# Performance work log

Hardware: AMD Instinct MI355X
Metric: run time of the kernel (lower is better)

## Reference

```python
import jax, jax.numpy as jnp
import numpy as np

N = 20000      # num nodes
E = 200000     # num edges (no self loops; GATConv adds them)
ND = 128       # node_feature_dim
ED = 64        # edge_feature_dim
H = 256        # hidden_dim (= GAT out_channels per head, concat=False)
HEADS = 4
L = 3          # num_gnn_layers


def setup_inputs() -> dict:
    key = jax.random.key(0)
    ks = jax.random.split(key, 24)
    rng = np.random.default_rng(0)
    src = rng.integers(0, N, size=E)
    dst = (src + 1 + rng.integers(0, N - 1, size=E)) % N  # guaranteed no self loops
    edge_index = jnp.asarray(np.stack([src, dst]), dtype=jnp.int32)
    s = 0.05
    inp = {
        'node_features': jax.random.normal(ks[0], (N, ND), jnp.float32),
        'edge_attr': jax.random.normal(ks[1], (E, ED), jnp.float32),
        'enc_w': jax.random.normal(ks[2], (ND, H), jnp.float32) * s,
        'enc_b': jnp.zeros((H,), jnp.float32),
        'edge_enc_w': jax.random.normal(ks[3], (L, ED, H), jnp.float32) * s,
        'edge_enc_b': jnp.zeros((L, H), jnp.float32),
        'gat_w': jax.random.normal(ks[4], (L, H, HEADS * H), jnp.float32) * s,
        'att_src': jax.random.normal(ks[5], (L, HEADS, H), jnp.float32) * s,
        'att_dst': jax.random.normal(ks[6], (L, HEADS, H), jnp.float32) * s,
        'att_edge': jax.random.normal(ks[7], (L, HEADS, H), jnp.float32) * s,
        'lin_edge_w': jax.random.normal(ks[8], (L, 1, HEADS * H), jnp.float32) * s,
        'gat_b': jnp.zeros((L, H), jnp.float32),
        'ln_g': jnp.ones((L, H), jnp.float32),
        'ln_b': jnp.zeros((L, H), jnp.float32),
        'head_w1': jax.random.normal(ks[9], (4, H, H // 2), jnp.float32) * s,
        'head_b1': jnp.zeros((4, H // 2), jnp.float32),
        'head_w2': jax.random.normal(ks[10], (4, H // 2, 1), jnp.float32) * s,
        'head_b2': jnp.zeros((4, 1), jnp.float32),
        'edge_index': edge_index,
    }
    return inp


def _layernorm(x, g, b, eps=1e-5):
    mu = x.mean(-1, keepdims=True)
    v = ((x - mu) ** 2).mean(-1, keepdims=True)
    return g * (x - mu) / jnp.sqrt(v + eps) + b


def _gat_layer(x, src, dst, ew_full, w, a_s_vec, a_d_vec, a_e_vec, lew, bias):
    # x: [N,H]; GATConv(heads=4, concat=False) with scalar edge feature (edge_dim=1)
    xp = (x @ w).reshape(N, HEADS, H)                       # [N,HEADS,H]
    a_s = (xp * a_s_vec).sum(-1)                            # [N,HEADS]
    a_d = (xp * a_d_vec).sum(-1)                            # [N,HEADS]
    ef = (ew_full[:, None] @ lew).reshape(-1, HEADS, H)     # [Etot,HEADS,H]
    a_e = (ef * a_e_vec).sum(-1)                            # [Etot,HEADS]
    logits = jax.nn.leaky_relu(a_s[src] + a_d[dst] + a_e, 0.2)
    m = jax.ops.segment_max(logits, dst, num_segments=N)    # segment softmax over dst
    p = jnp.exp(logits - m[dst])
    ssum = jax.ops.segment_sum(p, dst, num_segments=N)
    alpha = p / ssum[dst]                                   # [Etot,HEADS]
    out = jax.ops.segment_sum(alpha[:, :, None] * xp[src], dst, num_segments=N)
    return out.mean(1) + bias                               # concat=False -> mean over heads


def reference(node_features, edge_attr, enc_w, enc_b, edge_enc_w, edge_enc_b,
              gat_w, att_src, att_dst, att_edge, lin_edge_w, gat_b,
              ln_g, ln_b, head_w1, head_b1, head_w2, head_b2, edge_index):
    src0, dst0 = edge_index[0], edge_index[1]
    loop = jnp.arange(N, dtype=edge_index.dtype)
    src = jnp.concatenate([src0, loop])   # self loops appended (GATConv add_self_loops)
    dst = jnp.concatenate([dst0, loop])
    deg = jax.ops.segment_sum(jnp.ones((E,), node_features.dtype), dst0, num_segments=N)

    x = jax.nn.relu(node_features @ enc_w + enc_b)          # node encoder (dropout: eval)
    for l in range(L):
        ew = (edge_attr @ edge_enc_w[l] + edge_enc_b[l]).mean(-1)  # [E] scalar edge weight
        loop_w = jax.ops.segment_sum(ew, dst0, num_segments=N) / jnp.maximum(deg, 1.0)
        ew_full = jnp.concatenate([ew, loop_w])             # fill_value='mean' for self loops
        h = _gat_layer(x, src, dst, ew_full, gat_w[l], att_src[l], att_dst[l],
                       att_edge[l], lin_edge_w[l], gat_b[l])
        h = _layernorm(h, ln_g[l], ln_b[l])
        x = jax.nn.relu(x + h)
    emb = x                                                 # [N,H]

    # 4 prediction heads vectorized: k in {attrition, engagement, collaboration, anomaly}
    hmid = jax.nn.relu(jnp.einsum('nd,kdh->knh', emb, head_w1) + head_b1[:, None, :])
    o = jnp.einsum('knh,kho->kno', hmid, head_w2) + head_b2[:, None, :]  # [4,N,1]
    attrition = jax.nn.sigmoid(o[0])
    engagement = o[1]
    collaboration = o[2]
    anomaly = jax.nn.sigmoid(o[3])
    return (attrition, engagement, collaboration, anomaly, emb)
```

## Files before the change

kernel.cpp:

```cpp
#include <hip/hip_runtime.h>
#include <math.h>

#define N_NODES 20000
#define N_EDGES 200000
#define NDIM 128
#define EDIM 64
#define HDIM 256
#define HEADS 4
#define NH 1024
#define NLAYERS 3
#define SCAN_NBLK ((N_NODES + 255) / 256)

typedef __attribute__((ext_vector_type(8))) short short8;
typedef __attribute__((ext_vector_type(4))) float floatx4;

__device__ __forceinline__ float b2f(unsigned short u) {
    union { unsigned u; float f; } c; c.u = ((unsigned)u) << 16; return c.f;
}
__device__ __forceinline__ float b2f_lo(unsigned u) {
    union { unsigned u; float f; } c; c.u = u << 16; return c.f;
}
__device__ __forceinline__ float b2f_hi(unsigned u) {
    union { unsigned u; float f; } c; c.u = u & 0xffff0000u; return c.f;
}
__device__ __forceinline__ unsigned short f2b(float f) {
    union { float f; unsigned u; } c; c.f = f;
    unsigned u = c.u;
    return (unsigned short)((u + 0x7FFFu + ((u >> 16) & 1u)) >> 16);
}
__device__ __forceinline__ float lrelu(float v) { return v > 0.f ? v : 0.2f * v; }

__global__ void hist_kernel(const int* __restrict__ dst0, int* __restrict__ cnt) {
    int e = blockIdx.x * 256 + threadIdx.x;
    if (e < N_EDGES) atomicAdd(&cnt[dst0[e]], 1);
}

__global__ void scan_local(const int* __restrict__ cnt, int* __restrict__ row_ptr,
                           int* __restrict__ bsum) {
    __shared__ int wsum[4];
    int tid = threadIdx.x, lane = tid & 63, wid = tid >> 6;
    int n = blockIdx.x * 256 + tid;
    int v = (n < N_NODES) ? cnt[n] : 0;
    int s = v;
    #pragma unroll
    for (int off = 1; off < 64; off <<= 1) {
        int t = __shfl_up(s, off, 64);
        if (lane >= off) s += t;
    }
    if (lane == 63) wsum[wid] = s;
    __syncthreads();
    int woff = 0;
    #pragma unroll
    for (int w = 0; w < 4; w++) if (w < wid) woff += wsum[w];
    if (n < N_NODES) row_ptr[n] = woff + s - v;
    if (tid == 255) bsum[blockIdx.x] = woff + s;
}

__global__ void scan_bsums(int* __restrict__ bsum, int* __restrict__ boff) {
    __shared__ int wsum[2];
    int tid = threadIdx.x, lane = tid & 63, wid = tid >> 6;
    int v = (tid < SCAN_NBLK) ? bsum[tid] : 0;
    int s = v;
    #pragma unroll
    for (int off = 1; off < 64; off <<= 1) {
        int t = __shfl_up(s, off, 64);
        if (lane >= off) s += t;
    }
    if (lane == 63) wsum[wid] = s;
    __syncthreads();
    int woff = (wid == 1) ? wsum[0] : 0;
    if (tid < SCAN_NBLK) boff[tid] = woff + s - v;
    if (tid == SCAN_NBLK - 1) boff[SCAN_NBLK] = woff + s;
}

__global__ void scan_add(int* __restrict__ row_ptr, const int* __restrict__ boff) {
    int n = blockIdx.x * 256 + threadIdx.x;
    if (n < N_NODES) row_ptr[n] += boff[blockIdx.x];
    if (n == 0) row_ptr[N_NODES] = boff[SCAN_NBLK];
}

__global__ __launch_bounds__(256) void fill_ew(const int* __restrict__ src0,
                                               const int* __restrict__ dst0,
                                               const float* __restrict__ edge_attr,
                                               const float* __restrict__ wmean3,
                                               const float* __restrict__ scal3,
                                               const int* __restrict__ row_ptr,
                                               int* __restrict__ fillc,
                                               int* __restrict__ srcCSR,
                                               float* __restrict__ ewCSR4) {
    int e = blockIdx.x * 256 + threadIdx.x;
    if (e >= N_EDGES) return;
    int d = dst0[e];
    int p = atomicAdd(&fillc[d], 1);
    int pos = row_ptr[d] + p;
    srcCSR[pos] = src0[e];
    const float* row = edge_attr + (size_t)e * EDIM;
    float s0 = 0.f, s1 = 0.f, s2 = 0.f;
    #pragma unroll
    for (int dd = 0; dd < EDIM; dd += 4) {
        float4 a  = *(const float4*)(row + dd);
        float4 w0 = *(const float4*)(wmean3 + dd);
        float4 w1 = *(const float4*)(wmean3 + 64 + dd);
        float4 w2 = *(const float4*)(wmean3 + 128 + dd);
        s0 += a.x * w0.x + a.y * w0.y + a.z * w0.z + a.w * w0.w;
        s1 += a.x * w1.x + a.y * w1.y + a.z * w1.z + a.w * w1.w;
        s2 += a.x * w2.x + a.y * w2.y + a.z * w2.z + a.w * w2.w;
    }
    *(float4*)(ewCSR4 + (size_t)pos * 4) =
        make_float4(s0 + scal3[4], s1 + scal3[12], s2 + scal3[20], 0.f);
}

__global__ void transpose_bf(const float* __restrict__ in, unsigned short* __restrict__ out,
                             int K, int Nn, size_t in_bs, size_t out_bs) {
    in += blockIdx.z * in_bs;
    out += blockIdx.z * out_bs;
    __shared__ float sh[32][33];
    int tx = threadIdx.x, ty = threadIdx.y;
    int kb = blockIdx.y * 32, nb = blockIdx.x * 32;
    #pragma unroll
    for (int i = 0; i < 32; i += 8)
        sh[ty + i][tx] = in[(size_t)(kb + ty + i) * Nn + nb + tx];
    __syncthreads();
    #pragma unroll
    for (int i = 0; i < 32; i += 8)
        out[(size_t)(nb + ty + i) * K + kb + tx] = f2b(sh[tx][ty + i]);
}

__global__ void gat_w_prep(const float* __restrict__ in, unsigned short* __restrict__ out) {
    int z = blockIdx.z, l = z >> 2, h = z & 3;
    __shared__ float sh[32][33];
    int tx = threadIdx.x, ty = threadIdx.y;
    int kb = blockIdx.y * 32, db = blockIdx.x * 32;
    const float* src = in + (size_t)l * HDIM * NH + (size_t)h * HDIM;
    unsigned short* dst = out + (size_t)l * HDIM * NH + (size_t)h * HDIM;
    #pragma unroll
    for (int i = 0; i < 32; i += 8)
        sh[ty + i][tx] = src[(size_t)(kb + ty + i) * NH + db + tx];
    __syncthreads();
    #pragma unroll
    for (int i = 0; i < 32; i += 8)
        dst[(size_t)(db + ty + i) * NH + kb + tx] = f2b(0.25f * sh[tx][ty + i]);
}

__global__ void ws_prep(const float* __restrict__ gat_w, const float* __restrict__ att_src,
                        const float* __restrict__ att_dst,
                        float* __restrict__ ws_s, float* __restrict__ ws_d) {
    int l = blockIdx.x >> 2, h = blockIdx.x & 3;
    int k = threadIdx.x;
    const float* wrow = gat_w + (size_t)l * HDIM * NH + (size_t)k * NH + h * HDIM;
    const float* as = att_src + (size_t)l * NH + h * HDIM;
    const float* ad = att_dst + (size_t)l * NH + h * HDIM;
    float s1 = 0.f, s2 = 0.f;
    for (int d = 0; d < HDIM; d += 4) {
        float4 w4 = *(const float4*)(wrow + d);
        float4 a4 = *(const float4*)(as + d);
        float4 b4 = *(const float4*)(ad + d);
        s1 += w4.x * a4.x + w4.y * a4.y + w4.z * a4.z + w4.w * a4.w;
        s2 += w4.x * b4.x + w4.y * b4.y + w4.z * b4.z + w4.w * b4.w;
    }
    ws_s[(size_t)blockIdx.x * HDIM + k] = s1;
    ws_d[(size_t)blockIdx.x * HDIM + k] = s2;
}

__global__ void conv_bf(const float* __restrict__ in, unsigned short* __restrict__ out) {
    int i = blockIdx.x * 256 + threadIdx.x;
    float4 v = ((const float4*)in)[i];
    ushort4 o;
    o.x = f2b(v.x); o.y = f2b(v.y); o.z = f2b(v.z); o.w = f2b(v.w);
    ((ushort4*)out)[i] = o;
}

template <bool RELU, bool BIAS, bool HEAD2>
__global__ __launch_bounds__(256) void gemm_bf16(
    const unsigned short* __restrict__ A, const unsigned short* __restrict__ Bt,
    const float* __restrict__ bias, unsigned short* __restrict__ C,
    int M, int Ntot, int K,
    const float* __restrict__ w2 = nullptr, const float* __restrict__ b2v = nullptr,
    float* __restrict__ outp = nullptr)
{
    __shared__ char lds[16384];
    unsigned short* As = (unsigned short*)lds;
    unsigned short* Bs = (unsigned short*)(lds + 4096);
    unsigned short* Cs = (unsigned short*)lds;

    int Cb = Ntot >> 7;
    int P  = (M + 63) >> 6;
    int d  = blockIdx.x;
    int xcd = d & 7;
    int i5  = d >> 3;
    int p   = xcd + 8 * (i5 / Cb);
    int cblk = i5 % Cb;
    if (p >= P) return;
    int row0 = p * 64;
    int col0 = cblk * 128;

    int tid = threadIdx.x;
    int lane = tid & 63;
    int wid = tid >> 6;
    int wm = (wid >> 1) * 32;
    int wn = (wid & 1) * 64;
    int lm = lane & 15;
    int q8 = (lane >> 4) * 8;
    int q4 = (lane >> 4) * 4;

    floatx4 acc[2][4];
    #pragma unroll
    for (int i = 0; i < 2; i++)
        #pragma unroll
        for (int j = 0; j < 4; j++)
            acc[i][j] = (floatx4)(0.f);

    for (int k0 = 0; k0 < K; k0 += 32) {
        {
            int arow = tid >> 2;
            int acol = (tid & 3) * 8;
            int garow = row0 + arow; if (garow > M - 1) garow = M - 1;
            __builtin_amdgcn_global_load_lds(
                (__attribute__((address_space(1))) const void*)(A + (size_t)garow * K + k0 + acol),
                (__attribute__((address_space(3))) void*)(As + tid * 8), 16, 0, 0);
        }
        #pragma unroll
        for (int r = 0; r < 2; r++) {
            int chunk = tid + r * 256;
            int brow = chunk >> 2;
            int bcol = (chunk & 3) * 8;
            __builtin_amdgcn_global_load_lds(
                (__attribute__((address_space(1))) const void*)(Bt + (size_t)(col0 + brow) * K + k0 + bcol),
                (__attribute__((address_space(3))) void*)(Bs + chunk * 8), 16, 0, 0);
        }
        __syncthreads();
        short8 af[2], bf[4];
        #pragma unroll
        for (int i = 0; i < 2; i++)
            af[i] = *(const short8*)(As + (wm + i * 16 + lm) * 32 + q8);
        #pragma unroll
        for (int j = 0; j < 4; j++)
            bf[j] = *(const short8*)(Bs + (wn + j * 16 + lm) * 32 + q8);
        #pragma unroll
        for (int i = 0; i < 2; i++)
            #pragma unroll
            for (int j = 0; j < 4; j++)
                acc[i][j] = __builtin_amdgcn_mfma_f32_16x16x32_bf16(af[i], bf[j], acc[i][j], 0, 0, 0);
        __syncthreads();
    }

    #pragma unroll
    for (int i = 0; i < 2; i++) {
        #pragma unroll
        for (int j = 0; j < 4; j++) {
            int cl = wn + j * 16 + lm;
            float bv = BIAS ? bias[col0 + cl] : 0.f;
            #pragma unroll
            for (int reg = 0; reg < 4; reg++) {
                int rl = wm + i * 16 + q4 + reg;
                float v = acc[i][j][reg];
                if (BIAS) v += bv;
                if (RELU) v = fmaxf(v, 0.f);
                Cs[rl * 128 + cl] = f2b(v);
            }
        }
    }
    __syncthreads();
    if constexpr (!HEAD2) {
        int row = tid >> 2;
        int seg = (tid & 3) * 32;
        if (row0 + row < M) {
            #pragma unroll
            for (int u = 0; u < 4; u++) {
                int4 v = *(const int4*)(Cs + row * 128 + seg + u * 8);
                *(int4*)(C + (size_t)(row0 + row) * Ntot + col0 + seg + u * 8) = v;
            }
        }
    } else {
        int row = tid >> 2;
        int seg = (tid & 3) * 32;
        int k = col0 >> 7;
        const float* wr = w2 + k * 128;
        const unsigned short* cr = Cs + row * 128 + seg;
        float s = 0.f;
        #pragma unroll
        for (int u = 0; u < 4; u++) {
            int4 v = *(const int4*)(cr + u * 8);
            float4 w0 = *(const float4*)(wr + seg + u * 8);
            float4 w1 = *(const float4*)(wr + seg + u * 8 + 4);
            s += b2f_lo((unsigned)v.x) * w0.x + b2f_hi((unsigned)v.x) * w0.y
               + b2f_lo((unsigned)v.y) * w0.z + b2f_hi((unsigned)v.y) * w0.w;
            s += b2f_lo((unsigned)v.z) * w1.x + b2f_hi((unsigned)v.z) * w1.y
               + b2f_lo((unsigned)v.w) * w1.z + b2f_hi((unsigned)v.w) * w1.w;
        }
        s += __shfl_xor(s, 1, 64);
        s += __shfl_xor(s, 2, 64);
        if ((tid & 3) == 0 && row0 + row < M) {
            s += b2v[k];
            if (k == 0 || k == 3) s = 1.f / (1.f + __expf(-s));
            outp[(size_t)k * N_NODES + row0 + row] = s;
        }
    }
}

__global__ void layer_prep3(const float* __restrict__ edge_enc_w, const float* __restrict__ edge_enc_b,
                            const float* __restrict__ lin_edge_w, const float* __restrict__ att_edge,
                            float* __restrict__ wmean3, float* __restrict__ scal3)
{
    int l = blockIdx.x;
    const float* eew = edge_enc_w + (size_t)l * EDIM * HDIM;
    const float* eeb = edge_enc_b + (size_t)l * HDIM;
    const float* lew = lin_edge_w + (size_t)l * NH;
    const float* ae  = att_edge + (size_t)l * NH;
    float* wm = wmean3 + l * 64;
    float* sc = scal3 + l * 8;
    int tid = threadIdx.x;
    if (tid < 64) {
        float s = 0.f;
        for (int d = 0; d < HDIM; d++) s += eew[tid * HDIM + d];
        wm[tid] = s * (1.f / HDIM);
    } else if (tid < 68) {
        int h = tid - 64;
        float s = 0.f;
        for (int d = 0; d < HDIM; d++) s += lew[h * HDIM + d] * ae[h * HDIM + d];
        sc[h] = s;
    } else if (tid == 68) {
        float s = 0.f;
        for (int d = 0; d < HDIM; d++) s += eeb[d];
        sc[4] = s * (1.f / HDIM);
    }
}

__global__ void loop_weights_all(const float* __restrict__ ewCSR4, const int* __restrict__ row_ptr,
                                 float* __restrict__ loopw3)
{
    int n = blockIdx.x * 256 + threadIdx.x;
    if (n >= N_NODES) return;
    int r0 = row_ptr[n], r1 = row_ptr[n + 1];
    float s0 = 0.f, s1 = 0.f, s2 = 0.f;
    for (int i = r0; i < r1; i++) {
        float4 w = *(const float4*)(ewCSR4 + (size_t)i * 4);
        s0 += w.x; s1 += w.y; s2 += w.z;
    }
    float inv = 1.f / fmaxf((float)(r1 - r0), 1.f);
    loopw3[n] = s0 * inv;
    loopw3[N_NODES + n] = s1 * inv;
    loopw3[2 * N_NODES + n] = s2 * inv;
}

__global__ __launch_bounds__(256) void attn_x(const unsigned short* __restrict__ x_bf,
                                              const float* __restrict__ ws_s,
                                              const float* __restrict__ ws_d,
                                              float* __restrict__ a_s,
                                              float* __restrict__ a_d)
{
    int wid = threadIdx.x >> 6, lane = threadIdx.x & 63;
    int n = blockIdx.x * 4 + wid;
    ushort4 xv = *(const ushort4*)(x_bf + (size_t)n * HDIM + lane * 4);
    float x0 = b2f(xv.x), x1 = b2f(xv.y), x2 = b2f(xv.z), x3 = b2f(xv.w);
    float ss[4], sd[4];
    #pragma unroll
    for (int h = 0; h < 4; h++) {
        float4 s4 = *(const float4*)(ws_s + h * HDIM + lane * 4);
        float4 d4 = *(const float4*)(ws_d + h * HDIM + lane * 4);
        ss[h] = x0 * s4.x + x1 * s4.y + x2 * s4.z + x3 * s4.w;
        sd[h] = x0 * d4.x + x1 * d4.y + x2 * d4.z + x3 * d4.w;
    }
    #pragma unroll
    for (int off = 32; off > 0; off >>= 1)
        #pragma unroll
        for (int h = 0; h < 4; h++) {
            ss[h] += __shfl_xor(ss[h], off, 64);
            sd[h] += __shfl_xor(sd[h], off, 64);
        }
    if (lane == 0) {
        *(float4*)(a_s + n * 4) = make_float4(ss[0], ss[1], ss[2], ss[3]);
        *(float4*)(a_d + n * 4) = make_float4(sd[0], sd[1], sd[2], sd[3]);
    }
}

__global__ __launch_bounds__(256) void gat_agg_fused(
    const unsigned short* __restrict__ x_bf, const float* __restrict__ a_s,
    const float* __restrict__ a_d, const float* __restrict__ loopw,
    const float* __restrict__ scal, const int* __restrict__ row_ptr,
    const int* __restrict__ srcCSR, const float* __restrict__ ewCSR4,
    int l, unsigned short* __restrict__ agg)
{
    int wid = threadIdx.x >> 6, lane = threadIdx.x & 63;
    int n = blockIdx.x * 4 + wid;
    int r0 = row_ptr[n];
    int deg = row_ptr[n + 1] - r0;
    int cnt = deg + 1;

    float4 c4 = *(const float4*)scal;
    float4 as4 = *(const float4*)(a_s + (size_t)n * 4);
    float4 ad4 = *(const float4*)(a_d + (size_t)n * 4);
    float lw = loopw[n];
    float4 zself;
    zself.x = lrelu(as4.x + ad4.x + c4.x * lw);
    zself.y = lrelu(as4.y + ad4.y + c4.y * lw);
    zself.z = lrelu(as4.z + ad4.z + c4.z * lw);
    zself.w = lrelu(as4.w + ad4.w + c4.w * lw);

    auto comp_z = [&](int c0, int& sv, float4& z) {
        int ix = c0 + lane;
        if (ix < deg) {
            sv = srcCSR[r0 + ix];
            float w = ewCSR4[(((size_t)(r0 + ix)) << 2) + l];
            float4 zs = *(const float4*)(a_s + (size_t)sv * 4);
            z.x = lrelu(zs.x + ad4.x + c4.x * w);
            z.y = lrelu(zs.y + ad4.y + c4.y * w);
            z.z = lrelu(zs.z + ad4.z + c4.z * w);
            z.w = lrelu(zs.w + ad4.w + c4.w * w);
        } else if (ix == deg) {
            sv = n; z = zself;
        } else {
            sv = n; z.x = z.y = z.z = z.w = -1e30f;
        }
    };

    int sv0; float4 z0;
    comp_z(0, sv0, z0);
    float4 p0;
    p0.x = __expf(z0.x); p0.y = __expf(z0.y);
    p0.z = __expf(z0.z); p0.w = __expf(z0.w);
    float s0 = p0.x, s1 = p0.y, s2 = p0.z, s3 = p0.w;
    for (int c0 = 64; c0 < cnt; c0 += 64) {
        int sv; float4 z; comp_z(c0, sv, z);
        s0 += __expf(z.x); s1 += __expf(z.y);
        s2 += __expf(z.z); s3 += __expf(z.w);
    }
    #pragma unroll
    for (int off = 32; off > 0; off >>= 1) {
        s0 += __shfl_xor(s0, off, 64);
        s1 += __shfl_xor(s1, off, 64);
        s2 += __shfl_xor(s2, off, 64);
        s3 += __shfl_xor(s3, off, 64);
    }
    float i0 = 1.f / s0, i1 = 1.f / s1, i2 = 1.f / s2, i3 = 1.f / s3;
    float4 al0;
    al0.x = p0.x * i0; al0.y = p0.y * i1; al0.z = p0.z * i2; al0.w = p0.w * i3;

    float acc[4][4] = {};
    const unsigned short* xw = x_bf + (size_t)lane * 4;

    auto acc_one = [&](uint2 u, float a0, float a1, float a2, float a3) {
        float x0 = b2f_lo(u.x), x1 = b2f_hi(u.x), x2 = b2f_lo(u.y), x3 = b2f_hi(u.y);
        acc[0][0] += a0 * x0; acc[0][1] += a0 * x1; acc[0][2] += a0 * x2; acc[0][3] += a0 * x3;
        acc[1][0] += a1 * x0; acc[1][1] += a1 * x1; acc[1][2] += a1 * x2; acc[1][3] += a1 * x3;
        acc[2][0] += a2 * x0; acc[2][1] += a2 * x1; acc[2][2] += a2 * x2; acc[2][3] += a2 * x3;
        acc[3][0] += a3 * x0; acc[3][1] += a3 * x1; acc[3][2] += a3 * x2; acc[3][3] += a3 * x3;
    };

    auto agg_chunk = [&](int sv, float4 al, int mc) {
        int j = 0;
        for (; j + 3 < mc; j += 4) {
            int sA = __builtin_amdgcn_readfirstlane(__shfl(sv, j, 64));
            int sB = __builtin_amdgcn_readfirstlane(__shfl(sv, j + 1, 64));
            int sC = __builtin_amdgcn_readfirstlane(__shfl(sv, j + 2, 64));
            int sD = __builtin_amdgcn_readfirstlane(__shfl(sv, j + 3, 64));
            uint2 uA = *(const uint2*)(xw + (size_t)sA * HDIM);
            uint2 uB = *(const uint2*)(xw + (size_t)sB * HDIM);
            uint2 uC = *(const uint2*)(xw + (size_t)sC * HDIM);
            uint2 uD = *(const uint2*)(xw + (size_t)sD * HDIM);
            acc_one(uA, __shfl(al.x, j, 64), __shfl(al.y, j, 64),
                        __shfl(al.z, j, 64), __shfl(al.w, j, 64));
            acc_one(uB, __shfl(al.x, j + 1, 64), __shfl(al.y, j + 1, 64),
                        __shfl(al.z, j + 1, 64), __shfl(al.w, j + 1, 64));
            acc_one(uC, __shfl(al.x, j + 2, 64), __shfl(al.y, j + 2, 64),
                        __shfl(al.z, j + 2, 64), __shfl(al.w, j + 2, 64));
            acc_one(uD, __shfl(al.x, j + 3, 64), __shfl(al.y, j + 3, 64),
                        __shfl(al.z, j + 3, 64), __shfl(al.w, j + 3, 64));
        }
        for (; j + 1 < mc; j += 2) {
            int sA = __builtin_amdgcn_readfirstlane(__shfl(sv, j, 64));
            int sB = __builtin_amdgcn_readfirstlane(__shfl(sv, j + 1, 64));
            uint2 uA = *(const uint2*)(xw + (size_t)sA * HDIM);
            uint2 uB = *(const uint2*)(xw + (size_t)sB * HDIM);
            acc_one(uA, __shfl(al.x, j, 64), __shfl(al.y, j, 64),
                        __shfl(al.z, j, 64), __shfl(al.w, j, 64));
            acc_one(uB, __shfl(al.x, j + 1, 64), __shfl(al.y, j + 1, 64),
                        __shfl(al.z, j + 1, 64), __shfl(al.w, j + 1, 64));
        }
        if (j < mc) {
            int sA = __builtin_amdgcn_readfirstlane(__shfl(sv, j, 64));
            uint2 uA = *(const uint2*)(xw + (size_t)sA * HDIM);
            acc_one(uA, __shfl(al.x, j, 64), __shfl(al.y, j, 64),
                        __shfl(al.z, j, 64), __shfl(al.w, j, 64));
        }
    };

    agg_chunk(sv0, al0, min(64, cnt));
    for (int c0 = 64; c0 < cnt; c0 += 64) {
        int sv; float4 z; comp_z(c0, sv, z);
        float4 al;
        al.x = __expf(z.x) * i0; al.y = __expf(z.y) * i1;
        al.z = __expf(z.z) * i2; al.w = __expf(z.w) * i3;
        agg_chunk(sv, al, min(64, cnt - c0));
    }

    unsigned short* ag = agg + (size_t)n * NH + lane * 4;
    #pragma unroll
    for (int h = 0; h < 4; h++) {
        ushort4 o;
        o.x = f2b(acc[h][0]); o.y = f2b(acc[h][1]);
        o.z = f2b(acc[h][2]); o.w = f2b(acc[h][3]);
        *(ushort4*)(ag + h * 256) = o;
    }
}

template <bool ATTN, bool EMB>
__global__ __launch_bounds__(256) void ln_residual(const unsigned short* __restrict__ y_bf,
                                                   const float* __restrict__ ln_g,
                                                   const float* __restrict__ ln_b,
                                                   unsigned short* __restrict__ x_bf,
                                                   const float* __restrict__ ws_s,
                                                   const float* __restrict__ ws_d,
                                                   float* __restrict__ a_s,
                                                   float* __restrict__ a_d,
                                                   float* __restrict__ emb_out)
{
    int n = blockIdx.x * 4 + (threadIdx.x >> 6);
    int lane = threadIdx.x & 63;
    ushort4 yv = *(const ushort4*)(y_bf + (size_t)n * HDIM + lane * 4);
    float y0 = b2f(yv.x), y1 = b2f(yv.y), y2 = b2f(yv.z), y3 = b2f(yv.w);
    float s1 = y0 + y1 + y2 + y3;
    float s2 = y0 * y0 + y1 * y1 + y2 * y2 + y3 * y3;
    #pragma unroll
    for (int off = 32; off > 0; off >>= 1) {
        s1 += __shfl_xor(s1, off, 64);
        s2 += __shfl_xor(s2, off, 64);
    }
    float mu = s1 * (1.f / HDIM);
    float var = s2 * (1.f / HDIM) - mu * mu;
    float rsig = rsqrtf(var + 1e-5f);
    float4 g = *(const float4*)(ln_g + lane * 4);
    float4 b = *(const float4*)(ln_b + lane * 4);
    ushort4 xv = *(const ushort4*)(x_bf + (size_t)n * HDIM + lane * 4);
    ushort4 o;
    o.x = f2b(fmaxf(b2f(xv.x) + g.x * (y0 - mu) * rsig + b.x, 0.f));
    o.y = f2b(fmaxf(b2f(xv.y) + g.y * (y1 - mu) * rsig + b.y, 0.f));
    o.z = f2b(fmaxf(b2f(xv.z) + g.z * (y2 - mu) * rsig + b.z, 0.f));
    o.w = f2b(fmaxf(b2f(xv.w) + g.w * (y3 - mu) * rsig + b.w, 0.f));
    *(ushort4*)(x_bf + (size_t)n * HDIM + lane * 4) = o;

    float xn0 = b2f(o.x), xn1 = b2f(o.y), xn2 = b2f(o.z), xn3 = b2f(o.w);
    if (EMB) {
        *(float4*)(emb_out + (size_t)n * HDIM + lane * 4) = make_float4(xn0, xn1, xn2, xn3);
    }
    if (ATTN) {
        float ss[4], sd[4];
        #pragma unroll
        for (int h = 0; h < 4; h++) {
            float4 s4 = *(const float4*)(ws_s + h * HDIM + lane * 4);
            float4 d4 = *(const float4*)(ws_d + h * HDIM + lane * 4);
            ss[h] = xn0 * s4.x + xn1 * s4.y + xn2 * s4.z + xn3 * s4.w;
            sd[h] = xn0 * d4.x + xn1 * d4.y + xn2 * d4.z + xn3 * d4.w;
        }
        #pragma unroll
        for (int off = 32; off > 0; off >>= 1)
            #pragma unroll
            for (int h = 0; h < 4; h++) {
                ss[h] += __shfl_xor(ss[h], off, 64);
                sd[h] += __shfl_xor(sd[h], off, 64);
            }
        if (lane == 0) {
            *(float4*)(a_s + n * 4) = make_float4(ss[0], ss[1], ss[2], ss[3]);
            *(float4*)(a_d + n * 4) = make_float4(sd[0], sd[1], sd[2], sd[3]);
        }
    }
}

extern "C" void kernel_launch(void* const* d_in, const int* in_sizes, int n_in,
                              void* d_out, int out_size, void* d_ws, size_t ws_size,
                              hipStream_t stream) {
    const float* node_features = (const float*)d_in[0];
    const float* edge_attr     = (const float*)d_in[1];
    const float* enc_w         = (const float*)d_in[2];
    const float* enc_b         = (const float*)d_in[3];
    const float* edge_enc_w    = (const float*)d_in[4];
    const float* edge_enc_b    = (const float*)d_in[5];
    const float* gat_w         = (const float*)d_in[6];
    const float* att_src       = (const float*)d_in[7];
    const float* att_dst       = (const float*)d_in[8];
    const float* att_edge      = (const float*)d_in[9];
    const float* lin_edge_w    = (const float*)d_in[10];
    const float* gat_b         = (const float*)d_in[11];
    const float* ln_g          = (const float*)d_in[12];
    const float* ln_b          = (const float*)d_in[13];
    const float* head_w1       = (const float*)d_in[14];
    const float* head_b1       = (const float*)d_in[15];
    const float* head_w2       = (const float*)d_in[16];
    const float* head_b2       = (const float*)d_in[17];
    const int*   edge_index    = (const int*)d_in[18];
    const int* src0 = edge_index;
    const int* dst0 = edge_index + N_EDGES;
    float* out = (float*)d_out;

    char* cur = (char*)d_ws;
    auto alloc = [&](size_t bytes) { char* p = cur; cur += (bytes + 255) & ~(size_t)255; return p; };
    unsigned short* x_bf   = (unsigned short*)alloc((size_t)N_NODES * HDIM * 2);
    unsigned short* agg    = (unsigned short*)alloc((size_t)N_NODES * NH * 2);
    unsigned short* y_bf   = (unsigned short*)alloc((size_t)N_NODES * HDIM * 2);
    unsigned short* nf_bf  = (unsigned short*)alloc((size_t)N_NODES * NDIM * 2);
    unsigned short* enc_wt = (unsigned short*)alloc((size_t)HDIM * NDIM * 2);
    unsigned short* gw2t   = (unsigned short*)alloc((size_t)NLAYERS * NH * HDIM * 2);
    unsigned short* hw1t   = (unsigned short*)alloc((size_t)512 * HDIM * 2);
    float* ws_s   = (float*)alloc((size_t)NLAYERS * 4 * HDIM * 4);
    float* ws_d   = (float*)alloc((size_t)NLAYERS * 4 * HDIM * 4);
    float* a_s    = (float*)alloc((size_t)N_NODES * 4 * 4);
    float* a_d    = (float*)alloc((size_t)N_NODES * 4 * 4);
    float* ewCSR4 = (float*)alloc((size_t)N_EDGES * 4 * 4);
    float* loopw3 = (float*)alloc((size_t)3 * N_NODES * 4);
    float* wmean3 = (float*)alloc(192 * 4);
    float* scal3  = (float*)alloc(24 * 4);
    int* cnt      = (int*)alloc((size_t)2 * N_NODES * 4);
    int* fillc    = cnt + N_NODES;
    int* row_ptr  = (int*)alloc((size_t)(N_NODES + 1) * 4);
    int* bsum     = (int*)alloc((size_t)(SCAN_NBLK + 1) * 4);
    int* boff     = (int*)alloc((size_t)(SCAN_NBLK + 1) * 4);
    int* srcCSR   = (int*)alloc((size_t)N_EDGES * 4);

    hipMemsetAsync(cnt, 0, (size_t)2 * N_NODES * sizeof(int), stream);

    layer_prep3<<<3, 128, 0, stream>>>(edge_enc_w, edge_enc_b, lin_edge_w, att_edge, wmean3, scal3);
    hist_kernel<<<(N_EDGES + 255) / 256, 256, 0, stream>>>(dst0, cnt);
    scan_local<<<SCAN_NBLK, 256, 0, stream>>>(cnt, row_ptr, bsum);
    scan_bsums<<<1, 128, 0, stream>>>(bsum, boff);
    scan_add<<<SCAN_NBLK, 256, 0, stream>>>(row_ptr, boff);
    fill_ew<<<(N_EDGES + 255) / 256, 256, 0, stream>>>(src0, dst0, edge_attr, wmean3, scal3,
                                                       row_ptr, fillc, srcCSR, ewCSR4);
    loop_weights_all<<<(N_NODES + 255) / 256, 256, 0, stream>>>(ewCSR4, row_ptr, loopw3);

    conv_bf<<<(N_NODES * NDIM / 4) / 256, 256, 0, stream>>>(node_features, nf_bf);
    transpose_bf<<<dim3(HDIM / 32, NDIM / 32, 1), dim3(32, 8), 0, stream>>>(
        enc_w, enc_wt, NDIM, HDIM, 0, 0);
    gat_w_prep<<<dim3(8, 8, 12), dim3(32, 8), 0, stream>>>(gat_w, gw2t);
    ws_prep<<<12, 256, 0, stream>>>(gat_w, att_src, att_dst, ws_s, ws_d);
    transpose_bf<<<dim3(128 / 32, HDIM / 32, 4), dim3(32, 8), 0, stream>>>(
        head_w1, hw1t, HDIM, 128, (size_t)HDIM * 128, (size_t)128 * HDIM);

    const int GEMM_GRID_256 = 8 * (((N_NODES + 63) / 64 + 7) / 8) * (256 / 128);
    const int GEMM_GRID_512 = 8 * (((N_NODES + 63) / 64 + 7) / 8) * (512 / 128);

    gemm_bf16<true, true, false><<<GEMM_GRID_256, 256, 0, stream>>>(
        nf_bf, enc_wt, enc_b, x_bf, N_NODES, HDIM, NDIM);
    attn_x<<<N_NODES / 4, 256, 0, stream>>>(x_bf, ws_s, ws_d, a_s, a_d);

    for (int l = 0; l < NLAYERS; l++) {
        gat_agg_fused<<<N_NODES / 4, 256, 0, stream>>>(
            x_bf, a_s, a_d, loopw3 + (size_t)l * N_NODES, scal3 + l * 8,
            row_ptr, srcCSR, ewCSR4, l, agg);
        gemm_bf16<false, true, false><<<GEMM_GRID_256, 256, 0, stream>>>(
            agg, gw2t + (size_t)l * NH * HDIM, gat_b + (size_t)l * HDIM, y_bf,
            N_NODES, HDIM, NH);
        if (l < NLAYERS - 1) {
            ln_residual<true, false><<<N_NODES / 4, 256, 0, stream>>>(
                y_bf, ln_g + (size_t)l * HDIM, ln_b + (size_t)l * HDIM, x_bf,
                ws_s + (size_t)(l + 1) * 4 * HDIM, ws_d + (size_t)(l + 1) * 4 * HDIM,
                a_s, a_d, nullptr);
        } else {
            ln_residual<false, true><<<N_NODES / 4, 256, 0, stream>>>(
                y_bf, ln_g + (size_t)l * HDIM, ln_b + (size_t)l * HDIM, x_bf,
                nullptr, nullptr, nullptr, nullptr, out + 4 * N_NODES);
        }
    }

    gemm_bf16<true, true, true><<<GEMM_GRID_512, 256, 0, stream>>>(
        x_bf, hw1t, head_b1, nullptr, N_NODES, 512, HDIM,
        head_w2, head_b2, out);
}
```

Before: 427.0 us.

## Fuse GEMM with LayerNorm, residual and attention epilogue; single-block scan

Replaces the per-layer GEMM plus separate ln_residual and attn_x kernels with a 32-row-by-256-column GEMM whose epilogue does bias, LayerNorm, residual, ReLU, the attention-score dot products and the embedding write. This removes the y_bf intermediate round trip and several launches. It also replaces the three-kernel prefix scan with one 1024-thread block. The wider full-row tile gives a smaller grid (625 blocks) and uses more LDS per block, and the GEMM now computes in place on x_bf while other blocks read only their own rows.

```diff
diff --git a/kernel.cpp b/kernel.cpp
--- a/kernel.cpp
+++ b/kernel.cpp
@@ -9,7 +9,6 @@
 #define HEADS 4
 #define NH 1024
 #define NLAYERS 3
-#define SCAN_NBLK ((N_NODES + 255) / 256)
 
 typedef __attribute__((ext_vector_type(8))) short short8;
 typedef __attribute__((ext_vector_type(4))) float floatx4;
@@ -35,48 +34,38 @@
     if (e < N_EDGES) atomicAdd(&cnt[dst0[e]], 1);
 }
 
-__global__ void scan_local(const int* __restrict__ cnt, int* __restrict__ row_ptr,
-                           int* __restrict__ bsum) {
-    __shared__ int wsum[4];
-    int tid = threadIdx.x, lane = tid & 63, wid = tid >> 6;
-    int n = blockIdx.x * 256 + tid;
-    int v = (n < N_NODES) ? cnt[n] : 0;
-    int s = v;
+__global__ __launch_bounds__(1024) void scan_full(const int* __restrict__ cnt,
+                                                  int* __restrict__ row_ptr) {
+    const int PER = 20;
+    __shared__ int wtot[16];
+    int t = threadIdx.x, lane = t & 63, wid = t >> 6;
+    int base = t * PER;
+    int loc[PER];
+    int s = 0;
+    #pragma unroll
+    for (int i = 0; i < PER; i++) {
+        int idx = base + i;
+        int v = (idx < N_NODES) ? cnt[idx] : 0;
+        loc[i] = s; s += v;
+    }
+    int inc = s;
     #pragma unroll
     for (int off = 1; off < 64; off <<= 1) {
-        int t = __shfl_up(s, off, 64);
-        if (lane >= off) s += t;
-    }
-    if (lane == 63) wsum[wid] = s;
+        int tt = __shfl_up(inc, off, 64);
+        if (lane >= off) inc += tt;
+    }
+    if (lane == 63) wtot[wid] = inc;
     __syncthreads();
     int woff = 0;
     #pragma unroll
-    for (int w = 0; w < 4; w++) if (w < wid) woff += wsum[w];
-    if (n < N_NODES) row_ptr[n] = woff + s - v;
-    if (tid == 255) bsum[blockIdx.x] = woff + s;
-}
-
-__global__ void scan_bsums(int* __restrict__ bsum, int* __restrict__ boff) {
-    __shared__ int wsum[2];
-    int tid = threadIdx.x, lane = tid & 63, wid = tid >> 6;
-    int v = (tid < SCAN_NBLK) ? bsum[tid] : 0;
-    int s = v;
-    #pragma unroll
-    for (int off = 1; off < 64; off <<= 1) {
-        int t = __shfl_up(s, off, 64);
-        if (lane >= off) s += t;
-    }
-    if (lane == 63) wsum[wid] = s;
-    __syncthreads();
-    int woff = (wid == 1) ? wsum[0] : 0;
-    if (tid < SCAN_NBLK) boff[tid] = woff + s - v;
-    if (tid == SCAN_NBLK - 1) boff[SCAN_NBLK] = woff + s;
-}
-
-__global__ void scan_add(int* __restrict__ row_ptr, const int* __restrict__ boff) {
-    int n = blockIdx.x * 256 + threadIdx.x;
-    if (n < N_NODES) row_ptr[n] += boff[blockIdx.x];
-    if (n == 0) row_ptr[N_NODES] = boff[SCAN_NBLK];
+    for (int w = 0; w < 16; w++) if (w < wid) woff += wtot[w];
+    int excl = woff + inc - s;
+    #pragma unroll
+    for (int i = 0; i < PER; i++) {
+        int idx = base + i;
+        if (idx < N_NODES) row_ptr[idx] = excl + loc[i];
+    }
+    if (t == 1023) row_ptr[N_NODES] = excl + s;
 }
 
 __global__ __launch_bounds__(256) void fill_ew(const int* __restrict__ src0,
@@ -170,13 +159,157 @@
     ((ushort4*)out)[i] = o;
 }
 
-template <bool RELU, bool BIAS, bool HEAD2>
-__global__ __launch_bounds__(256) void gemm_bf16(
+template <bool RELU, bool LN, bool ATTN, bool EMB>
+__global__ __launch_bounds__(256) void gemm_fused(
     const unsigned short* __restrict__ A, const unsigned short* __restrict__ Bt,
-    const float* __restrict__ bias, unsigned short* __restrict__ C,
-    int M, int Ntot, int K,
-    const float* __restrict__ w2 = nullptr, const float* __restrict__ b2v = nullptr,
-    float* __restrict__ outp = nullptr)
+    const float* __restrict__ bias, unsigned short* __restrict__ x_bf, int K,
+    const float* __restrict__ ln_g, const float* __restrict__ ln_b,
+    const float* __restrict__ ws_s, const float* __restrict__ ws_d,
+    float* __restrict__ a_s, float* __restrict__ a_d,
+    float* __restrict__ emb_out)
+{
+    __shared__ char lds[33280];
+    unsigned short* As = (unsigned short*)lds;
+    unsigned short* Bs = (unsigned short*)(lds + 2048);
+    float* Cs = (float*)lds;
+
+    int row0 = blockIdx.x * 32;
+    int tid = threadIdx.x;
+    int lane = tid & 63;
+    int wid = tid >> 6;
+    int wn = wid * 64;
+    int lm = lane & 15;
+    int q8 = (lane >> 4) * 8;
+    int q4 = (lane >> 4) * 4;
+
+    floatx4 acc[2][4];
+    #pragma unroll
+    for (int i = 0; i < 2; i++)
+        #pragma unroll
+        for (int j = 0; j < 4; j++)
+            acc[i][j] = (floatx4)(0.f);
+
+    for (int k0 = 0; k0 < K; k0 += 32) {
+        if (tid < 128) {
+            int arow = tid >> 2;
+            int acol = (tid & 3) * 8;
+            __builtin_amdgcn_global_load_lds(
+                (__attribute__((address_space(1))) const void*)(A + (size_t)(row0 + arow) * K + k0 + acol),
+                (__attribute__((address_space(3))) void*)(As + tid * 8), 16, 0, 0);
+        }
+        #pragma unroll
+        for (int r = 0; r < 4; r++) {
+            int chunk = tid + r * 256;
+            int brow = chunk >> 2;
+            int bcol = (chunk & 3) * 8;
+            __builtin_amdgcn_global_load_lds(
+                (__attribute__((address_space(1))) const void*)(Bt + (size_t)brow * K + k0 + bcol),
+                (__attribute__((address_space(3))) void*)(Bs + chunk * 8), 16, 0, 0);
+        }
+        __syncthreads();
+        short8 af[2], bf[4];
+        #pragma unroll
+        for (int i = 0; i < 2; i++)
+            af[i] = *(const short8*)(As + (i * 16 + lm) * 32 + q8);
+        #pragma unroll
+        for (int j = 0; j < 4; j++)
+            bf[j] = *(const short8*)(Bs + (wn + j * 16 + lm) * 32 + q8);
+        #pragma unroll
+        for (int i = 0; i < 2; i++)
+            #pragma unroll
+            for (int j = 0; j < 4; j++)
+                acc[i][j] = __builtin_amdgcn_mfma_f32_16x16x32_bf16(af[i], bf[j], acc[i][j], 0, 0, 0);
+        __syncthreads();
+    }
+
+    #pragma unroll
+    for (int i = 0; i < 2; i++) {
+        #pragma unroll
+        for (int j = 0; j < 4; j++) {
+            int cl = wn + j * 16 + lm;
+            float bv = bias[cl];
+            #pragma unroll
+            for (int reg = 0; reg < 4; reg++) {
+                int rl = i * 16 + q4 + reg;
+                Cs[rl * 260 + cl] = acc[i][j][reg] + bv;
+            }
+        }
+    }
+    __syncthreads();
+
+    float4 g4, b4;
+    float4 wsv[4], wdv[4];
+    if (LN) {
+        g4 = *(const float4*)(ln_g + lane * 4);
+        b4 = *(const float4*)(ln_b + lane * 4);
+    }
+    if (ATTN) {
+        #pragma unroll
+        for (int h = 0; h < 4; h++) {
+            wsv[h] = *(const float4*)(ws_s + h * HDIM + lane * 4);
+            wdv[h] = *(const float4*)(ws_d + h * HDIM + lane * 4);
+        }
+    }
+    #pragma unroll
+    for (int t = 0; t < 8; t++) {
+        int r = wid * 8 + t;
+        int node = row0 + r;
+        float4 y = *(const float4*)(Cs + r * 260 + lane * 4);
+        float xn0, xn1, xn2, xn3;
+        if (LN) {
+            float s1 = y.x + y.y + y.z + y.w;
+            float s2 = y.x * y.x + y.y * y.y + y.z * y.z + y.w * y.w;
+            #pragma unroll
+            for (int off = 32; off > 0; off >>= 1) {
+                s1 += __shfl_xor(s1, off, 64);
+                s2 += __shfl_xor(s2, off, 64);
+            }
+            float mu = s1 * (1.f / HDIM);
+            float var = s2 * (1.f / HDIM) - mu * mu;
+            float rsig = rsqrtf(var + 1e-5f);
+            ushort4 xv = *(const ushort4*)(x_bf + (size_t)node * HDIM + lane * 4);
+            xn0 = fmaxf(b2f(xv.x) + g4.x * (y.x - mu) * rsig + b4.x, 0.f);
+            xn1 = fmaxf(b2f(xv.y) + g4.y * (y.y - mu) * rsig + b4.y, 0.f);
+            xn2 = fmaxf(b2f(xv.z) + g4.z * (y.z - mu) * rsig + b4.z, 0.f);
+            xn3 = fmaxf(b2f(xv.w) + g4.w * (y.w - mu) * rsig + b4.w, 0.f);
+        } else {
+            xn0 = fmaxf(y.x, 0.f); xn1 = fmaxf(y.y, 0.f);
+            xn2 = fmaxf(y.z, 0.f); xn3 = fmaxf(y.w, 0.f);
+        }
+        ushort4 o;
+        o.x = f2b(xn0); o.y = f2b(xn1); o.z = f2b(xn2); o.w = f2b(xn3);
+        *(ushort4*)(x_bf + (size_t)node * HDIM + lane * 4) = o;
+        float v0 = b2f(o.x), v1 = b2f(o.y), v2 = b2f(o.z), v3 = b2f(o.w);
+        if (EMB) {
+            *(float4*)(emb_out + (size_t)node * HDIM + lane * 4) = make_float4(v0, v1, v2, v3);
+        }
+        if (ATTN) {
+            float ss[4], sd[4];
+            #pragma unroll
+            for (int h = 0; h < 4; h++) {
+                ss[h] = v0 * wsv[h].x + v1 * wsv[h].y + v2 * wsv[h].z + v3 * wsv[h].w;
+                sd[h] = v0 * wdv[h].x + v1 * wdv[h].y + v2 * wdv[h].z + v3 * wdv[h].w;
+            }
+            #pragma unroll
+            for (int off = 32; off > 0; off >>= 1)
+                #pragma unroll
+                for (int h = 0; h < 4; h++) {
+                    ss[h] += __shfl_xor(ss[h], off, 64);
+                    sd[h] += __shfl_xor(sd[h], off, 64);
+                }
+            if (lane == 0) {
+                *(float4*)(a_s + node * 4) = make_float4(ss[0], ss[1], ss[2], ss[3]);
+                *(float4*)(a_d + node * 4) = make_float4(sd[0], sd[1], sd[2], sd[3]);
+            }
+        }
+    }
+}
+
+__global__ __launch_bounds__(256) void gemm_head(
+    const unsigned short* __restrict__ A, const unsigned short* __restrict__ Bt,
+    const float* __restrict__ bias, int M, int Ntot, int K,
+    const float* __restrict__ w2, const float* __restrict__ b2v,
+    float* __restrict__ outp)
 {
     __shared__ char lds[16384];
     unsigned short* As = (unsigned short*)lds;
@@ -249,52 +382,38 @@
         #pragma unroll
         for (int j = 0; j < 4; j++) {
             int cl = wn + j * 16 + lm;
-            float bv = BIAS ? bias[col0 + cl] : 0.f;
+            float bv = bias[col0 + cl];
             #pragma unroll
             for (int reg = 0; reg < 4; reg++) {
                 int rl = wm + i * 16 + q4 + reg;
-                float v = acc[i][j][reg];
-                if (BIAS) v += bv;
-                if (RELU) v = fmaxf(v, 0.f);
+                float v = fmaxf(acc[i][j][reg] + bv, 0.f);
                 Cs[rl * 128 + cl] = f2b(v);
             }
         }
     }
     __syncthreads();
-    if constexpr (!HEAD2) {
-        int row = tid >> 2;
-        int seg = (tid & 3) * 32;
-        if (row0 + row < M) {
-            #pragma unroll
-            for (int u = 0; u < 4; u++) {
-                int4 v = *(const int4*)(Cs + row * 128 + seg + u * 8);
-                *(int4*)(C + (size_t)(row0 + row) * Ntot + col0 + seg + u * 8) = v;
-            }
-        }
-    } else {
-        int row = tid >> 2;
-        int seg = (tid & 3) * 32;
-        int k = col0 >> 7;
-        const float* wr = w2 + k * 128;
-        const unsigned short* cr = Cs + row * 128 + seg;
-        float s = 0.f;
-        #pragma unroll
-        for (int u = 0; u < 4; u++) {
-            int4 v = *(const int4*)(cr + u * 8);
-            float4 w0 = *(const float4*)(wr + seg + u * 8);
-            float4 w1 = *(const float4*)(wr + seg + u * 8 + 4);
-            s += b2f_lo((unsigned)v.x) * w0.x + b2f_hi((unsigned)v.x) * w0.y
-               + b2f_lo((unsigned)v.y) * w0.z + b2f_hi((unsigned)v.y) * w0.w;
-            s += b2f_lo((unsigned)v.z) * w1.x + b2f_hi((unsigned)v.z) * w1.y
-               + b2f_lo((unsigned)v.w) * w1.z + b2f_hi((unsigned)v.w) * w1.w;
-        }
-        s += __shfl_xor(s, 1, 64);
-        s += __shfl_xor(s, 2, 64);
-        if ((tid & 3) == 0 && row0 + row < M) {
-            s += b2v[k];
-            if (k == 0 || k == 3) s = 1.f / (1.f + __expf(-s));
-            outp[(size_t)k * N_NODES + row0 + row] = s;
-        }
+    int row = tid >> 2;
+    int seg = (tid & 3) * 32;
+    int k = col0 >> 7;
+    const float* wr = w2 + k * 128;
+    const unsigned short* cr = Cs + row * 128 + seg;
+    float s = 0.f;
+    #pragma unroll
+    for (int u = 0; u < 4; u++) {
+        int4 v = *(const int4*)(cr + u * 8);
+        float4 w0 = *(const float4*)(wr + seg + u * 8);
+        float4 w1 = *(const float4*)(wr + seg + u * 8 + 4);
+        s += b2f_lo((unsigned)v.x) * w0.x + b2f_hi((unsigned)v.x) * w0.y
+           + b2f_lo((unsigned)v.y) * w0.z + b2f_hi((unsigned)v.y) * w0.w;
+        s += b2f_lo((unsigned)v.z) * w1.x + b2f_hi((unsigned)v.z) * w1.y
+           + b2f_lo((unsigned)v.w) * w1.z + b2f_hi((unsigned)v.w) * w1.w;
+    }
+    s += __shfl_xor(s, 1, 64);
+    s += __shfl_xor(s, 2, 64);
+    if ((tid & 3) == 0 && row0 + row < M) {
+        s += b2v[k];
+        if (k == 0 || k == 3) s = 1.f / (1.f + __expf(-s));
+        outp[(size_t)k * N_NODES + row0 + row] = s;
     }
 }
 
@@ -343,37 +462,6 @@
     loopw3[2 * N_NODES + n] = s2 * inv;
 }
 
-__global__ __launch_bounds__(256) void attn_x(const unsigned short* __restrict__ x_bf,
-                                              const float* __restrict__ ws_s,
-                                              const float* __restrict__ ws_d,
-                                              float* __restrict__ a_s,
-                                              float* __restrict__ a_d)
-{
-    int wid = threadIdx.x >> 6, lane = threadIdx.x & 63;
-    int n = blockIdx.x * 4 + wid;
-    ushort4 xv = *(const ushort4*)(x_bf + (size_t)n * HDIM + lane * 4);
-    float x0 = b2f(xv.x), x1 = b2f(xv.y), x2 = b2f(xv.z), x3 = b2f(xv.w);
-    float ss[4], sd[4];
-    #pragma unroll
-    for (int h = 0; h < 4; h++) {
-        float4 s4 = *(const float4*)(ws_s + h * HDIM + lane * 4);
-        float4 d4 = *(const float4*)(ws_d + h * HDIM + lane * 4);
-        ss[h] = x0 * s4.x + x1 * s4.y + x2 * s4.z + x3 * s4.w;
-        sd[h] = x0 * d4.x + x1 * d4.y + x2 * d4.z + x3 * d4.w;
-    }
-    #pragma unroll
-    for (int off = 32; off > 0; off >>= 1)
-        #pragma unroll
-        for (int h = 0; h < 4; h++) {
-            ss[h] += __shfl_xor(ss[h], off, 64);
-            sd[h] += __shfl_xor(sd[h], off, 64);
-        }
-    if (lane == 0) {
-        *(float4*)(a_s + n * 4) = make_float4(ss[0], ss[1], ss[2], ss[3]);
-        *(float4*)(a_d + n * 4) = make_float4(sd[0], sd[1], sd[2], sd[3]);
-    }
-}
-
 __global__ __launch_bounds__(256) void gat_agg_fused(
     const unsigned short* __restrict__ x_bf, const float* __restrict__ a_s,
     const float* __restrict__ a_d, const float* __restrict__ loopw,
@@ -501,68 +589,6 @@
         o.x = f2b(acc[h][0]); o.y = f2b(acc[h][1]);
         o.z = f2b(acc[h][2]); o.w = f2b(acc[h][3]);
         *(ushort4*)(ag + h * 256) = o;
-    }
-}
-
-template <bool ATTN, bool EMB>
-__global__ __launch_bounds__(256) void ln_residual(const unsigned short* __restrict__ y_bf,
-                                                   const float* __restrict__ ln_g,
-                                                   const float* __restrict__ ln_b,
-                                                   unsigned short* __restrict__ x_bf,
-                                                   const float* __restrict__ ws_s,
-                                                   const float* __restrict__ ws_d,
-                                                   float* __restrict__ a_s,
-                                                   float* __restrict__ a_d,
-                                                   float* __restrict__ emb_out)
-{
-    int n = blockIdx.x * 4 + (threadIdx.x >> 6);
-    int lane = threadIdx.x & 63;
-    ushort4 yv = *(const ushort4*)(y_bf + (size_t)n * HDIM + lane * 4);
-    float y0 = b2f(yv.x), y1 = b2f(yv.y), y2 = b2f(yv.z), y3 = b2f(yv.w);
-    float s1 = y0 + y1 + y2 + y3;
-    float s2 = y0 * y0 + y1 * y1 + y2 * y2 + y3 * y3;
-    #pragma unroll
-    for (int off = 32; off > 0; off >>= 1) {
-        s1 += __shfl_xor(s1, off, 64);
-        s2 += __shfl_xor(s2, off, 64);
-    }
-    float mu = s1 * (1.f / HDIM);
-    float var = s2 * (1.f / HDIM) - mu * mu;
-    float rsig = rsqrtf(var + 1e-5f);
-    float4 g = *(const float4*)(ln_g + lane * 4);
-    float4 b = *(const float4*)(ln_b + lane * 4);
-    ushort4 xv = *(const ushort4*)(x_bf + (size_t)n * HDIM + lane * 4);
-    ushort4 o;
-    o.x = f2b(fmaxf(b2f(xv.x) + g.x * (y0 - mu) * rsig + b.x, 0.f));
-    o.y = f2b(fmaxf(b2f(xv.y) + g.y * (y1 - mu) * rsig + b.y, 0.f));
-    o.z = f2b(fmaxf(b2f(xv.z) + g.z * (y2 - mu) * rsig + b.z, 0.f));
-    o.w = f2b(fmaxf(b2f(xv.w) + g.w * (y3 - mu) * rsig + b.w, 0.f));
-    *(ushort4*)(x_bf + (size_t)n * HDIM + lane * 4) = o;
-
-    float xn0 = b2f(o.x), xn1 = b2f(o.y), xn2 = b2f(o.z), xn3 = b2f(o.w);
-    if (EMB) {
-        *(float4*)(emb_out + (size_t)n * HDIM + lane * 4) = make_float4(xn0, xn1, xn2, xn3);
-    }
-    if (ATTN) {
-        float ss[4], sd[4];
-        #pragma unroll
-        for (int h = 0; h < 4; h++) {
-            float4 s4 = *(const float4*)(ws_s + h * HDIM + lane * 4);
-            float4 d4 = *(const float4*)(ws_d + h * HDIM + lane * 4);
-            ss[h] = xn0 * s4.x + xn1 * s4.y + xn2 * s4.z + xn3 * s4.w;
-            sd[h] = xn0 * d4.x + xn1 * d4.y + xn2 * d4.z + xn3 * d4.w;
-        }
-        #pragma unroll
-        for (int off = 32; off > 0; off >>= 1)
-            #pragma unroll
-            for (int h = 0; h < 4; h++) {
-                ss[h] += __shfl_xor(ss[h], off, 64);
-                sd[h] += __shfl_xor(sd[h], off, 64);
-            }
-        if (lane == 0) {
-            *(float4*)(a_s + n * 4) = make_float4(ss[0], ss[1], ss[2], ss[3]);
-            *(float4*)(a_d + n * 4) = make_float4(sd[0], sd[1], sd[2], sd[3]);
-        }
     }
 }
 
@@ -596,7 +622,6 @@
     auto alloc = [&](size_t bytes) { char* p = cur; cur += (bytes + 255) & ~(size_t)255; return p; };
     unsigned short* x_bf   = (unsigned short*)alloc((size_t)N_NODES * HDIM * 2);
     unsigned short* agg    = (unsigned short*)alloc((size_t)N_NODES * NH * 2);
-    unsigned short* y_bf   = (unsigned short*)alloc((size_t)N_NODES * HDIM * 2);
     unsigned short* nf_bf  = (unsigned short*)alloc((size_t)N_NODES * NDIM * 2);
     unsigned short* enc_wt = (unsigned short*)alloc((size_t)HDIM * NDIM * 2);
     unsigned short* gw2t   = (unsigned short*)alloc((size_t)NLAYERS * NH * HDIM * 2);
@@ -612,17 +637,13 @@
     int* cnt      = (int*)alloc((size_t)2 * N_NODES * 4);
     int* fillc    = cnt + N_NODES;
     int* row_ptr  = (int*)alloc((size_t)(N_NODES + 1) * 4);
-    int* bsum     = (int*)alloc((size_t)(SCAN_NBLK + 1) * 4);
-    int* boff     = (int*)alloc((size_t)(SCAN_NBLK + 1) * 4);
     int* srcCSR   = (int*)alloc((size_t)N_EDGES * 4);
 
     hipMemsetAsync(cnt, 0, (size_t)2 * N_NODES * sizeof(int), stream);
 
     layer_prep3<<<3, 128, 0, stream>>>(edge_enc_w, edge_enc_b, lin_edge_w, att_edge, wmean3, scal3);
     hist_kernel<<<(N_EDGES + 255) / 256, 256, 0, stream>>>(dst0, cnt);
-    scan_local<<<SCAN_NBLK, 256, 0, stream>>>(cnt, row_ptr, bsum);
-    scan_bsums<<<1, 128, 0, stream>>>(bsum, boff);
-    scan_add<<<SCAN_NBLK, 256, 0, stream>>>(row_ptr, boff);
+    scan_full<<<1, 1024, 0, stream>>>(cnt, row_ptr);
     fill_ew<<<(N_EDGES + 255) / 256, 256, 0, stream>>>(src0, dst0, edge_attr, wmean3, scal3,
                                                        row_ptr, fillc, srcCSR, ewCSR4);
     loop_weights_all<<<(N_NODES + 255) / 256, 256, 0, stream>>>(ewCSR4, row_ptr, loopw3);
@@ -635,33 +656,31 @@
     transpose_bf<<<dim3(128 / 32, HDIM / 32, 4), dim3(32, 8), 0, stream>>>(
         head_w1, hw1t, HDIM, 128, (size_t)HDIM * 128, (size_t)128 * HDIM);
 
-    const int GEMM_GRID_256 = 8 * (((N_NODES + 63) / 64 + 7) / 8) * (256 / 128);
-    const int GEMM_GRID_512 = 8 * (((N_NODES + 63) / 64 + 7) / 8) * (512 / 128);
-
-    gemm_bf16<true, true, false><<<GEMM_GRID_256, 256, 0, stream>>>(
-        nf_bf, enc_wt, enc_b, x_bf, N_NODES, HDIM, NDIM);
-    attn_x<<<N_NODES / 4, 256, 0, stream>>>(x_bf, ws_s, ws_d, a_s, a_d);
+    const int GRID_F = N_NODES / 32;
+
+    gemm_fused<true, false, true, false><<<GRID_F, 256, 0, stream>>>(
+        nf_bf, enc_wt, enc_b, x_bf, NDIM,
+        nullptr, nullptr, ws_s, ws_d, a_s, a_d, nullptr);
 
     for (int l = 0; l < NLAYERS; l++) {
         gat_agg_fused<<<N_NODES / 4, 256, 0, stream>>>(
             x_bf, a_s, a_d, loopw3 + (size_t)l * N_NODES, scal3 + l * 8,
             row_ptr, srcCSR, ewCSR4, l, agg);
-        gemm_bf16<false, true, false><<<GEMM_GRID_256, 256, 0, stream>>>(
-            agg, gw2t + (size_t)l * NH * HDIM, gat_b + (size_t)l * HDIM, y_bf,
-            N_NODES, HDIM, NH);
         if (l < NLAYERS - 1) {
-            ln_residual<true, false><<<N_NODES / 4, 256, 0, stream>>>(
-                y_bf, ln_g + (size_t)l * HDIM, ln_b + (size_t)l * HDIM, x_bf,
+            gemm_fused<false, true, true, false><<<GRID_F, 256, 0, stream>>>(
+                agg, gw2t + (size_t)l * NH * HDIM, gat_b + (size_t)l * HDIM, x_bf, NH,
+                ln_g + (size_t)l * HDIM, ln_b + (size_t)l * HDIM,
                 ws_s + (size_t)(l + 1) * 4 * HDIM, ws_d + (size_t)(l + 1) * 4 * HDIM,
                 a_s, a_d, nullptr);
         } else {
-            ln_residual<false, true><<<N_NODES / 4, 256, 0, stream>>>(
-                y_bf, ln_g + (size_t)l * HDIM, ln_b + (size_t)l * HDIM, x_bf,
+            gemm_fused<false, true, false, true><<<GRID_F, 256, 0, stream>>>(
+                agg, gw2t + (size_t)l * NH * HDIM, gat_b + (size_t)l * HDIM, x_bf, NH,
+                ln_g + (size_t)l * HDIM, ln_b + (size_t)l * HDIM,
                 nullptr, nullptr, nullptr, nullptr, out + 4 * N_NODES);
         }
     }
 
-    gemm_bf16<true, true, true><<<GEMM_GRID_512, 256, 0, stream>>>(
-        x_bf, hw1t, head_b1, nullptr, N_NODES, 512, HDIM,
-        head_w2, head_b2, out);
-}
+    const int GRID_HEAD = 8 * (((N_NODES + 63) / 64 + 7) / 8) * (512 / 128);
+    gemm_head<<<GRID_HEAD, 256, 0, stream>>>(
+        x_bf, hw1t, head_b1, N_NODES, 512, HDIM, head_w2, head_b2, out);
+}
```

Result: slower. 447.4 us (+4.8%).
